# Optimization experiments

Measured on AMD Instinct MI355X. Metric: run time of the kernel, lower is better.

## Reference

```python
import jax, jax.numpy as jnp
import numpy as np

N_ATOMS = 100000
N_BONDS = 250000
MAX_NB = 6
HIDDEN = 256
DEPTH = 3
NUM_MOLS = 2000
ATOM_FDIM = 133
BOND_FDIM = 147


def setup_inputs() -> dict:
    key = jax.random.key(0)
    ks = jax.random.split(key, 12)
    return {
        "f_atoms": jax.random.normal(ks[0], (N_ATOMS, ATOM_FDIM), jnp.float32),
        "f_bonds": jax.random.normal(ks[1], (N_BONDS, BOND_FDIM), jnp.float32),
        "w_atoms": jax.random.uniform(ks[2], (N_ATOMS,), jnp.float32),
        "w_bonds": jax.random.uniform(ks[3], (N_BONDS,), jnp.float32),
        "W_i": jax.random.normal(ks[4], (BOND_FDIM, HIDDEN), jnp.float32) * 0.05,
        "W_h": jax.random.normal(ks[5], (HIDDEN, HIDDEN), jnp.float32) * 0.05,
        "W_o": jax.random.normal(ks[6], (ATOM_FDIM + HIDDEN, HIDDEN), jnp.float32) * 0.05,
        "b_o": jnp.zeros((HIDDEN,), jnp.float32),
        "degree_of_polym": jax.random.uniform(ks[7], (NUM_MOLS,), jnp.float32),
        "a2b": jax.random.randint(ks[8], (N_ATOMS, MAX_NB), 0, N_BONDS, jnp.int32),
        "b2a": jax.random.randint(ks[9], (N_BONDS,), 0, N_ATOMS, jnp.int32),
        "b2revb": jax.random.randint(ks[10], (N_BONDS,), 0, N_BONDS, jnp.int32),
        "mol_ids": jnp.sort(jax.random.randint(ks[11], (N_ATOMS,), 0, NUM_MOLS, jnp.int32)),
    }


def reference(f_atoms, f_bonds, w_atoms, w_bonds, W_i, W_h, W_o, b_o,
              degree_of_polym, a2b, b2a, b2revb, mol_ids):
    # input-layer: bond features -> hidden messages
    inp = f_bonds @ W_i                      # [n_bonds, H]
    message = jax.nn.relu(inp)

    for _ in range(DEPTH - 1):
        # gather incoming bond messages per atom and weight them
        nei_msg = message[a2b]               # [n_atoms, max_nb, H]
        nei_w = w_bonds[a2b]                 # [n_atoms, max_nb]
        a_message = (nei_msg * nei_w[..., None]).sum(axis=1)  # [n_atoms, H]
        # directed message: total at source atom minus reverse bond
        message = a_message[b2a] - message[b2revb]             # [n_bonds, H]
        message = jax.nn.relu(inp + message @ W_h)             # dropout p=0 (eval)

    # final atom-level readout
    nei_msg = message[a2b] * w_bonds[a2b][..., None]
    a_message = nei_msg.sum(axis=1)                            # [n_atoms, H]
    a_input = jnp.concatenate([f_atoms, a_message], axis=1)    # [n_atoms, atom_fdim+H]
    atom_hiddens = jax.nn.relu(a_input @ W_o + b_o)            # [n_atoms, H]

    # per-molecule weighted mean aggregation (a_scope loop -> segment_sum)
    weighted = atom_hiddens * w_atoms[:, None]
    mol_sum = jax.ops.segment_sum(weighted, mol_ids, num_segments=NUM_MOLS)
    w_sum = jax.ops.segment_sum(w_atoms, mol_ids, num_segments=NUM_MOLS)
    safe_w = jnp.where(w_sum > 0, w_sum, 1.0)
    mol_vecs = jnp.where((w_sum > 0)[:, None], mol_sum / safe_w[:, None], 0.0)
    mol_vecs = degree_of_polym[:, None] * mol_vecs             # [num_mols, H]
    return mol_vecs
```

## Files before the change

### kernel.cpp

```cpp
#include <hip/hip_runtime.h>
#include <hip/hip_bf16.h>

typedef unsigned short u16;
typedef __bf16 bf16x8v __attribute__((ext_vector_type(8)));
typedef float f32x4v __attribute__((ext_vector_type(4)));
typedef float f32x4u __attribute__((ext_vector_type(4))) __attribute__((aligned(4)));

__device__ __forceinline__ float bf2f(u16 u) {
    union { float f; unsigned int i; } c; c.i = ((unsigned int)u) << 16; return c.f;
}
__device__ __forceinline__ u16 f2bf(float f) {
    union { float f; unsigned int i; } c; c.f = f;
    unsigned int i = c.i;
    unsigned int lsb = (i >> 16) & 1u;
    i += 0x7fffu + lsb;
    return (u16)(i >> 16);
}
__device__ __forceinline__ float lo16(unsigned u) { return bf2f((u16)(u & 0xffff)); }
__device__ __forceinline__ float hi16(unsigned u) { return bf2f((u16)(u >> 16)); }
__device__ __forceinline__ unsigned pack2(float lo, float hi) {
    return (unsigned)f2bf(lo) | ((unsigned)f2bf(hi) << 16);
}

__device__ __forceinline__ unsigned neg2(unsigned u) { return u ^ 0x80008000u; }
__device__ __forceinline__ unsigned relu_neg2(unsigned u) {
    unsigned s = u & 0x80008000u;
    unsigned m = (s - (s >> 15)) | s;
    return (u ^ 0x80008000u) & ~m;
}

__device__ __forceinline__ bf16x8v load_cvt8(const float* __restrict__ rowp, int k, int kmax) {
    union { unsigned u[4]; bf16x8v v; } r;
#pragma unroll
    for (int g = 0; g < 2; ++g) {
        int kk = k + g * 4;
        float f0, f1, f2, f3;
        if (kk + 3 < kmax) {
            f32x4u q = *(const f32x4u*)(rowp + kk);
            f0 = q.x; f1 = q.y; f2 = q.z; f3 = q.w;
        } else {
            f0 = (kk + 0 < kmax) ? rowp[kk + 0] : 0.f;
            f1 = (kk + 1 < kmax) ? rowp[kk + 1] : 0.f;
            f2 = (kk + 2 < kmax) ? rowp[kk + 2] : 0.f;
            f3 = (kk + 3 < kmax) ? rowp[kk + 3] : 0.f;
        }
        r.u[g * 2]     = pack2(f0, f1);
        r.u[g * 2 + 1] = pack2(f2, f3);
    }
    return r.v;
}

__global__ __launch_bounds__(256)
void pack_all(const float* __restrict__ W_i, const float* __restrict__ W_h,
              const float* __restrict__ W_o,
              u16* __restrict__ wti, u16* __restrict__ wth, u16* __restrict__ wto) {
    int idx = blockIdx.x * 256 + threadIdx.x;
    if (idx < 256 * 160) {
        int n = idx / 160, k = idx % 160;
        wti[idx] = f2bf(k < 147 ? W_i[k * 256 + n] : 0.f);
        return;
    }
    idx -= 256 * 160;
    if (idx < 256 * 256) {
        int n = idx / 256, k = idx % 256;
        wth[idx] = f2bf(W_h[k * 256 + n]);
        return;
    }
    idx -= 256 * 256;
    if (idx < 256 * 448) {
        int n = idx / 448, k = idx % 448;
        float v;
        if (k < 256)       v = W_o[(133 + k) * 256 + n];
        else if (k < 389)  v = W_o[(k - 256) * 256 + n];
        else               v = 0.f;
        wto[idx] = f2bf(v);
    }
}

template <bool RELU>
__global__ __launch_bounds__(256)
void gather16(const u16* __restrict__ msg, const int* __restrict__ a2b,
              const float* __restrict__ w_bonds, u16* __restrict__ out, int nAtoms) {
    int t = threadIdx.x;
    int g = t >> 5;
    int co = (t & 31) * 8;
    int atom0 = blockIdx.x * 16 + g;
    int atom1 = atom0 + 8;
    if (atom1 >= nAtoms) { if (atom0 >= nAtoms) return; atom1 = atom0; }

    int bidx[12];
#pragma unroll
    for (int j = 0; j < 6; ++j) {
        bidx[j]     = a2b[atom0 * 6 + j];
        bidx[6 + j] = a2b[atom1 * 6 + j];
    }
    float w[12];
#pragma unroll
    for (int j = 0; j < 12; ++j) w[j] = w_bonds[bidx[j]];
    uint4 v[12];
#pragma unroll
    for (int j = 0; j < 12; ++j)
        v[j] = *(const uint4*)(msg + (size_t)bidx[j] * 256 + co);

    float a0[8] = {0,0,0,0,0,0,0,0}, a1[8] = {0,0,0,0,0,0,0,0};
#pragma unroll
    for (int j = 0; j < 6; ++j) {
        unsigned p[4] = {v[j].x, v[j].y, v[j].z, v[j].w};
        unsigned q[4] = {v[6+j].x, v[6+j].y, v[6+j].z, v[6+j].w};
#pragma unroll
        for (int c = 0; c < 4; ++c) {
            float m0 = lo16(p[c]), m1 = hi16(p[c]);
            float n0 = lo16(q[c]), n1 = hi16(q[c]);
            if (RELU) {
                m0 = fmaxf(m0, 0.f); m1 = fmaxf(m1, 0.f);
                n0 = fmaxf(n0, 0.f); n1 = fmaxf(n1, 0.f);
            }
            a0[c * 2]     += w[j] * m0;
            a0[c * 2 + 1] += w[j] * m1;
            a1[c * 2]     += w[6+j] * n0;
            a1[c * 2 + 1] += w[6+j] * n1;
        }
    }
    uint4 o0, o1;
    o0.x = pack2(a0[0], a0[1]); o0.y = pack2(a0[2], a0[3]);
    o0.z = pack2(a0[4], a0[5]); o0.w = pack2(a0[6], a0[7]);
    o1.x = pack2(a1[0], a1[1]); o1.y = pack2(a1[2], a1[3]);
    o1.z = pack2(a1[4], a1[5]); o1.w = pack2(a1[6], a1[7]);
    *(uint4*)(out + (size_t)atom0 * 256 + co) = o0;
    if (atom1 != atom0)
        *(uint4*)(out + (size_t)atom1 * 256 + co) = o1;
}

__global__ __launch_bounds__(512, 2)
void gemm_in(const float* __restrict__ A, const u16* __restrict__ Bt, int M,
             u16* __restrict__ out0) {
    constexpr int KPAD = 160, KMAX = 147, ASTR = 147;
    constexpr int LSTR = KPAD + 8;
    __shared__ u16 Bs[256 * LSTR];
    const int tid = threadIdx.x;
    const int wave = tid >> 6;
    const int lane = tid & 63;
    const int mrow = lane & 15;
    const int quad = lane >> 4;

    constexpr int KC = KPAD / 8;
    for (int i = tid; i < 256 * KC; i += 512) {
        int r = i / KC, kc = i % KC;
        *(uint4*)&Bs[r * LSTR + kc * 8] = *(const uint4*)&Bt[(size_t)r * KPAD + kc * 8];
    }
    __syncthreads();

    for (long chunk = blockIdx.x; chunk * 256 < (long)M; chunk += gridDim.x) {
        const long mbase = chunk * 256 + wave * 32;
        const float* rowp[2];
#pragma unroll
        for (int t = 0; t < 2; ++t) {
            long r = mbase + t * 16 + mrow;
            if (r >= M) r = M - 1;
            rowp[t] = A + r * ASTR;
        }

        f32x4v acc[2][16];
#pragma unroll
        for (int t = 0; t < 2; ++t)
#pragma unroll
            for (int j = 0; j < 16; ++j) acc[t][j] = (f32x4v){0.f, 0.f, 0.f, 0.f};

#pragma unroll 2
        for (int k0 = 0; k0 < KPAD; k0 += 32) {
            bf16x8v a_frag[2];
#pragma unroll
            for (int t = 0; t < 2; ++t)
                a_frag[t] = load_cvt8(rowp[t], k0 + quad * 8, KMAX);
#pragma unroll
            for (int jg = 0; jg < 4; ++jg) {
                bf16x8v b_frag[4];
#pragma unroll
                for (int j4 = 0; j4 < 4; ++j4)
                    b_frag[j4] = *(const bf16x8v*)&Bs[((jg * 4 + j4) * 16 + mrow) * LSTR + k0 + quad * 8];
#pragma unroll
                for (int t = 0; t < 2; ++t)
#pragma unroll
                    for (int j4 = 0; j4 < 4; ++j4)
                        acc[t][jg * 4 + j4] = __builtin_amdgcn_mfma_f32_16x16x32_bf16(
                            a_frag[t], b_frag[j4], acc[t][jg * 4 + j4], 0, 0, 0);
            }
        }

#pragma unroll
        for (int t = 0; t < 2; ++t)
#pragma unroll
            for (int r = 0; r < 4; ++r) {
                long grow = mbase + t * 16 + quad * 4 + r;
                if (grow < M)
#pragma unroll
                    for (int j = 0; j < 16; ++j)
                        out0[(size_t)grow * 256 + j * 16 + mrow] = f2bf(acc[t][j][r]);
            }
    }
}

template <bool RELUV>
__global__ __launch_bounds__(512, 4)
void gemm_mp(const u16* __restrict__ amsg, const u16* __restrict__ msgsrc,
             const int* __restrict__ b2a, const int* __restrict__ b2revb,
             const u16* __restrict__ Bt, int M,
             const u16* __restrict__ inp, u16* __restrict__ out0) {
    constexpr int KPAD = 256;
    constexpr int LSTR = KPAD + 8;
    constexpr int NROWS = 128;
    __shared__ u16 Bs[NROWS * LSTR];
    const int tid = threadIdx.x;
    const int wave = tid >> 6;
    const int lane = tid & 63;
    const int mrow = lane & 15;
    const int quad = lane >> 4;

    const int nch = (M + 255) >> 8;
    const int cpx = (nch + 7) >> 3;
    const int bid = blockIdx.x;
    const int xcd = bid & 7;
    const int seq = bid >> 3;
    const long chunk = (long)xcd * cpx + (seq >> 1);
    if (chunk >= nch) return;
    const int nbase = (seq & 1) * NROWS;

    constexpr int KC = KPAD / 8;
    for (int i = tid; i < NROWS * KC; i += 512) {
        int r = i / KC, kc = i % KC;
        *(uint4*)&Bs[r * LSTR + kc * 8] = *(const uint4*)&Bt[(size_t)(nbase + r) * KPAD + kc * 8];
    }
    __syncthreads();

    const long mbase = chunk * 256 + wave * 32;
    size_t soff[2], roff[2];
#pragma unroll
    for (int t = 0; t < 2; ++t) {
        long b = mbase + t * 16 + mrow;
        if (b >= M) b = M - 1;
        soff[t] = (size_t)b2a[b] * 256 + quad * 8;
        roff[t] = (size_t)b2revb[b] * 256 + quad * 8;
    }

    f32x4v acc[2][8];
#pragma unroll
    for (int t = 0; t < 2; ++t)
#pragma unroll
        for (int j = 0; j < 8; ++j) acc[t][j] = (f32x4v){0.f, 0.f, 0.f, 0.f};

    uint4 va[2][2], vr[2][2];
#pragma unroll
    for (int t = 0; t < 2; ++t) {
        va[0][t] = *(const uint4*)&amsg[soff[t]];
        vr[0][t] = *(const uint4*)&msgsrc[roff[t]];
    }
#pragma unroll
    for (int kk = 0; kk < 8; ++kk) {
        const int k0 = kk * 32;
        const int cur = kk & 1, nxt = cur ^ 1;
        if (kk < 7) {
#pragma unroll
            for (int t = 0; t < 2; ++t) {
                va[nxt][t] = *(const uint4*)&amsg[soff[t] + k0 + 32];
                vr[nxt][t] = *(const uint4*)&msgsrc[roff[t] + k0 + 32];
            }
        }
        bf16x8v a1[2], a2[2];
#pragma unroll
        for (int t = 0; t < 2; ++t) {
            union { uint4 q; bf16x8v v; } ua, ur;
            ua.q = va[cur][t];
            uint4 w = vr[cur][t];
            if (RELUV) {
                ur.q.x = relu_neg2(w.x); ur.q.y = relu_neg2(w.y);
                ur.q.z = relu_neg2(w.z); ur.q.w = relu_neg2(w.w);
            } else {
                ur.q.x = neg2(w.x); ur.q.y = neg2(w.y);
                ur.q.z = neg2(w.z); ur.q.w = neg2(w.w);
            }
            a1[t] = ua.v;
            a2[t] = ur.v;
        }
#pragma unroll
        for (int jg = 0; jg < 2; ++jg) {
            bf16x8v b_frag[4];
#pragma unroll
            for (int j4 = 0; j4 < 4; ++j4)
                b_frag[j4] = *(const bf16x8v*)&Bs[((jg * 4 + j4) * 16 + mrow) * LSTR + k0 + quad * 8];
#pragma unroll
            for (int t = 0; t < 2; ++t)
#pragma unroll
                for (int j4 = 0; j4 < 4; ++j4) {
                    acc[t][jg * 4 + j4] = __builtin_amdgcn_mfma_f32_16x16x32_bf16(
                        a1[t], b_frag[j4], acc[t][jg * 4 + j4], 0, 0, 0);
                    acc[t][jg * 4 + j4] = __builtin_amdgcn_mfma_f32_16x16x32_bf16(
                        a2[t], b_frag[j4], acc[t][jg * 4 + j4], 0, 0, 0);
                }
        }
    }

#pragma unroll
    for (int t = 0; t < 2; ++t)
#pragma unroll
        for (int r = 0; r < 4; ++r) {
            long grow = mbase + t * 16 + quad * 4 + r;
            if (grow < M)
#pragma unroll
                for (int j = 0; j < 8; ++j) {
                    size_t idx = (size_t)grow * 256 + nbase + j * 16 + mrow;
                    float s = bf2f(inp[idx]) + acc[t][j][r];
                    out0[idx] = f2bf(s > 0.f ? s : 0.f);
                }
        }
}

__global__ __launch_bounds__(512, 2)
void gemm_ro(const u16* __restrict__ A1, const float* __restrict__ A2,
             const u16* __restrict__ Bt, int M,
             const float* __restrict__ bias, float* __restrict__ outf) {
    constexpr int KPAD = 448, KSPLIT = 256, K2 = 192, KMAX2 = 133;
    constexpr int LSTR = KPAD + 8;
    constexpr int NROWS = 128;
    __shared__ u16 Bs[NROWS * LSTR];
    const int tid = threadIdx.x;
    const int wave = tid >> 6;
    const int lane = tid & 63;
    const int mrow = lane & 15;
    const int quad = lane >> 4;

    const int nch = (M + 255) >> 8;
    const int cpx = (nch + 7) >> 3;
    const int bid = blockIdx.x;
    const int xcd = bid & 7;
    const int seq = bid >> 3;
    const long chunk = (long)xcd * cpx + (seq >> 1);
    if (chunk >= nch) return;
    const int nbase = (seq & 1) * NROWS;

    constexpr int KC = KPAD / 8;
    for (int i = tid; i < NROWS * KC; i += 512) {
        int r = i / KC, kc = i % KC;
        *(uint4*)&Bs[r * LSTR + kc * 8] =
            *(const uint4*)&Bt[(size_t)(nbase + r) * KPAD + kc * 8];
    }
    __syncthreads();

    const long mbase = chunk * 256 + wave * 32;
    long row[2];
#pragma unroll
    for (int t = 0; t < 2; ++t) {
        long r = mbase + t * 16 + mrow;
        if (r >= M) r = M - 1;
        row[t] = r;
    }

    f32x4v acc[2][8];
#pragma unroll
    for (int t = 0; t < 2; ++t)
#pragma unroll
        for (int j = 0; j < 8; ++j) acc[t][j] = (f32x4v){0.f, 0.f, 0.f, 0.f};

#pragma unroll 2
    for (int k0 = 0; k0 < KSPLIT; k0 += 32) {
        bf16x8v a_frag[2], b_frag[8];
#pragma unroll
        for (int t = 0; t < 2; ++t)
            a_frag[t] = *(const bf16x8v*)&A1[row[t] * KSPLIT + k0 + quad * 8];
#pragma unroll
        for (int j = 0; j < 8; ++j)
            b_frag[j] = *(const bf16x8v*)&Bs[(j * 16 + mrow) * LSTR + k0 + quad * 8];
#pragma unroll
        for (int t = 0; t < 2; ++t)
#pragma unroll
            for (int j = 0; j < 8; ++j)
                acc[t][j] = __builtin_amdgcn_mfma_f32_16x16x32_bf16(
                    a_frag[t], b_frag[j], acc[t][j], 0, 0, 0);
    }
#pragma unroll 2
    for (int k0 = 0; k0 < K2; k0 += 32) {
        bf16x8v a_frag[2], b_frag[8];
#pragma unroll
        for (int t = 0; t < 2; ++t)
            a_frag[t] = load_cvt8(A2 + row[t] * KMAX2, k0 + quad * 8, KMAX2);
#pragma unroll
        for (int j = 0; j < 8; ++j)
            b_frag[j] = *(const bf16x8v*)&Bs[(j * 16 + mrow) * LSTR + KSPLIT + k0 + quad * 8];
#pragma unroll
        for (int t = 0; t < 2; ++t)
#pragma unroll
            for (int j = 0; j < 8; ++j)
                acc[t][j] = __builtin_amdgcn_mfma_f32_16x16x32_bf16(
                    a_frag[t], b_frag[j], acc[t][j], 0, 0, 0);
    }

#pragma unroll
    for (int t = 0; t < 2; ++t)
#pragma unroll
        for (int r = 0; r < 4; ++r) {
            long grow = mbase + t * 16 + quad * 4 + r;
            if (grow < M)
#pragma unroll
                for (int j = 0; j < 8; ++j) {
                    int gcol = nbase + j * 16 + mrow;
                    float s = acc[t][j][r] + bias[gcol];
                    outf[(size_t)grow * 256 + gcol] = s > 0.f ? s : 0.f;
                }
        }
}

__global__ __launch_bounds__(256)
void aggregate_kernel(const float* __restrict__ hid, const float* __restrict__ w_atoms,
                      const int* __restrict__ mol_ids, const float* __restrict__ deg,
                      float* __restrict__ out, int nAtoms) {
    int m = blockIdx.x;
    int t = threadIdx.x;
    int lo = 0, hi = nAtoms;
    while (lo < hi) { int mid = (lo + hi) >> 1; if (mol_ids[mid] < m) lo = mid + 1; else hi = mid; }
    int start = lo;
    lo = start; hi = nAtoms;
    while (lo < hi) { int mid = (lo + hi) >> 1; if (mol_ids[mid] < m + 1) lo = mid + 1; else hi = mid; }
    int end = lo;
    float acc = 0.f, wsum = 0.f;
    for (int a = start; a < end; ++a) {
        float w = w_atoms[a];
        wsum += w;
        acc += w * hid[(size_t)a * 256 + t];
    }
    float res = (wsum > 0.f) ? deg[m] * acc / wsum : 0.f;
    out[m * 256 + t] = res;
}

extern "C" void kernel_launch(void* const* d_in, const int* in_sizes, int n_in,
                              void* d_out, int out_size, void* d_ws, size_t ws_size,
                              hipStream_t stream) {
    const float* f_atoms = (const float*)d_in[0];
    const float* f_bonds = (const float*)d_in[1];
    const float* w_atoms = (const float*)d_in[2];
    const float* w_bonds = (const float*)d_in[3];
    const float* W_i     = (const float*)d_in[4];
    const float* W_h     = (const float*)d_in[5];
    const float* W_o     = (const float*)d_in[6];
    const float* b_o     = (const float*)d_in[7];
    const float* deg     = (const float*)d_in[8];
    const int*   a2b     = (const int*)d_in[9];
    const int*   b2a     = (const int*)d_in[10];
    const int*   b2revb  = (const int*)d_in[11];
    const int*   mol_ids = (const int*)d_in[12];
    float* out = (float*)d_out;

    const int nB = 250000, nA = 100000, nM = 2000;

    char* ws = (char*)d_ws;
    u16* inp    = (u16*)(ws);
    u16* msgA   = (u16*)(ws + 128000000L);
    float* hid  = (float*)(ws + 256000000L);
    u16* amsg   = (u16*)(ws + 384000000L);
    u16* wt_i   = (u16*)(ws + 435200000L);
    u16* wt_h   = (u16*)(ws + 435200000L + 81920L);
    u16* wt_o   = (u16*)(ws + 435200000L + 81920L + 131072L);

    if (ws_size < 435642368UL) return;

    dim3 b256(256), b512(512);
    pack_all<<<dim3((256 * 160 + 256 * 256 + 256 * 448 + 255) / 256), b256, 0, stream>>>(
        W_i, W_h, W_o, wt_i, wt_h, wt_o);

    gemm_in<<<dim3(977), b512, 0, stream>>>(f_bonds, wt_i, nB, inp);

    const int nchB = (nB + 255) >> 8, cpxB = (nchB + 7) >> 3;
    dim3 gmp(8 * cpxB * 2);
    const int nchA = (nA + 255) >> 8, cpxA = (nchA + 7) >> 3;
    dim3 gro(8 * cpxA * 2);

    gather16<true><<<dim3((nA + 15) / 16), b256, 0, stream>>>(inp, a2b, w_bonds, amsg, nA);
    gemm_mp<true><<<gmp, b512, 0, stream>>>(
        amsg, inp, b2a, b2revb, wt_h, nB, inp, msgA);

    gather16<false><<<dim3((nA + 15) / 16), b256, 0, stream>>>(msgA, a2b, w_bonds, amsg, nA);
    gemm_mp<false><<<gmp, b512, 0, stream>>>(
        amsg, msgA, b2a, b2revb, wt_h, nB, inp, inp);

    gather16<false><<<dim3((nA + 15) / 16), b256, 0, stream>>>(inp , a2b, w_bonds, amsg, nA);
    gemm_ro<<<gro, b512, 0, stream>>>(amsg, f_atoms, wt_o, nA, b_o, hid);

    aggregate_kernel<<<dim3(nM), b256, 0, stream>>>(hid, w_atoms, mol_ids, deg, out, nA);
}
```

Measured before the change: 902.5 us.

## Retile message-passing GEMM to 1024-thread blocks holding all of W_h in LDS

Rewrites gemm_mp so each 1024-thread block stages the full 256x256 W_h in shared memory and covers 128 bond rows. Pairs of waves share a 16-row tile and each wave takes one half of the output columns. The XCD-aware chunk mapping and the register double-buffered prefetch of gathered rows are dropped in favour of a simple unroll-2 K loop. This halves per-wave accumulators and may raise latency hiding, but each LDS B fragment now feeds one row tile instead of two. Each block also copies twice as much weight data into LDS, and both waves in a pair gather the same A rows.

```diff
diff --git a/kernel.cpp b/kernel.cpp
--- a/kernel.cpp
+++ b/kernel.cpp
@@ -201,117 +201,70 @@
 }
 
 template <bool RELUV>
-__global__ __launch_bounds__(512, 4)
+__global__ __launch_bounds__(1024, 4)
 void gemm_mp(const u16* __restrict__ amsg, const u16* __restrict__ msgsrc,
              const int* __restrict__ b2a, const int* __restrict__ b2revb,
              const u16* __restrict__ Bt, int M,
              const u16* __restrict__ inp, u16* __restrict__ out0) {
     constexpr int KPAD = 256;
     constexpr int LSTR = KPAD + 8;
-    constexpr int NROWS = 128;
-    __shared__ u16 Bs[NROWS * LSTR];
+    __shared__ u16 Bs[256 * LSTR];
     const int tid = threadIdx.x;
     const int wave = tid >> 6;
     const int lane = tid & 63;
     const int mrow = lane & 15;
     const int quad = lane >> 4;
-
-    const int nch = (M + 255) >> 8;
-    const int cpx = (nch + 7) >> 3;
-    const int bid = blockIdx.x;
-    const int xcd = bid & 7;
-    const int seq = bid >> 3;
-    const long chunk = (long)xcd * cpx + (seq >> 1);
-    if (chunk >= nch) return;
-    const int nbase = (seq & 1) * NROWS;
-
-    constexpr int KC = KPAD / 8;
-    for (int i = tid; i < NROWS * KC; i += 512) {
-        int r = i / KC, kc = i % KC;
-        *(uint4*)&Bs[r * LSTR + kc * 8] = *(const uint4*)&Bt[(size_t)(nbase + r) * KPAD + kc * 8];
+    const int wgrp = wave >> 1;
+    const int nbase = (wave & 1) * 128;
+
+    for (int i = tid; i < 256 * 32; i += 1024) {
+        int r = i >> 5, kc = i & 31;
+        *(uint4*)&Bs[r * LSTR + kc * 8] = *(const uint4*)&Bt[(size_t)r * KPAD + kc * 8];
     }
     __syncthreads();
 
-    const long mbase = chunk * 256 + wave * 32;
-    size_t soff[2], roff[2];
-#pragma unroll
-    for (int t = 0; t < 2; ++t) {
-        long b = mbase + t * 16 + mrow;
-        if (b >= M) b = M - 1;
-        soff[t] = (size_t)b2a[b] * 256 + quad * 8;
-        roff[t] = (size_t)b2revb[b] * 256 + quad * 8;
-    }
-
-    f32x4v acc[2][8];
-#pragma unroll
-    for (int t = 0; t < 2; ++t)
-#pragma unroll
-        for (int j = 0; j < 8; ++j) acc[t][j] = (f32x4v){0.f, 0.f, 0.f, 0.f};
-
-    uint4 va[2][2], vr[2][2];
-#pragma unroll
-    for (int t = 0; t < 2; ++t) {
-        va[0][t] = *(const uint4*)&amsg[soff[t]];
-        vr[0][t] = *(const uint4*)&msgsrc[roff[t]];
-    }
-#pragma unroll
-    for (int kk = 0; kk < 8; ++kk) {
-        const int k0 = kk * 32;
-        const int cur = kk & 1, nxt = cur ^ 1;
-        if (kk < 7) {
-#pragma unroll
-            for (int t = 0; t < 2; ++t) {
-                va[nxt][t] = *(const uint4*)&amsg[soff[t] + k0 + 32];
-                vr[nxt][t] = *(const uint4*)&msgsrc[roff[t] + k0 + 32];
+    const long mbase = (long)blockIdx.x * 128 + wgrp * 16;
+    long b = mbase + mrow;
+    if (b >= M) b = M - 1;
+    const size_t soff = (size_t)b2a[b] * 256 + quad * 8;
+    const size_t roff = (size_t)b2revb[b] * 256 + quad * 8;
+
+    f32x4v acc[8];
+#pragma unroll
+    for (int j = 0; j < 8; ++j) acc[j] = (f32x4v){0.f, 0.f, 0.f, 0.f};
+
+#pragma unroll 2
+    for (int k0 = 0; k0 < KPAD; k0 += 32) {
+        uint4 va = *(const uint4*)&amsg[soff + k0];
+        uint4 vr = *(const uint4*)&msgsrc[roff + k0];
+        union { uint4 q; bf16x8v v; } ua, ur;
+        ua.q = va;
+        if (RELUV) {
+            ur.q.x = relu_neg2(vr.x); ur.q.y = relu_neg2(vr.y);
+            ur.q.z = relu_neg2(vr.z); ur.q.w = relu_neg2(vr.w);
+        } else {
+            ur.q.x = neg2(vr.x); ur.q.y = neg2(vr.y);
+            ur.q.z = neg2(vr.z); ur.q.w = neg2(vr.w);
+        }
+#pragma unroll
+        for (int j = 0; j < 8; ++j) {
+            bf16x8v b_frag = *(const bf16x8v*)&Bs[(nbase + j * 16 + mrow) * LSTR + k0 + quad * 8];
+            acc[j] = __builtin_amdgcn_mfma_f32_16x16x32_bf16(ua.v, b_frag, acc[j], 0, 0, 0);
+            acc[j] = __builtin_amdgcn_mfma_f32_16x16x32_bf16(ur.v, b_frag, acc[j], 0, 0, 0);
+        }
+    }
+
+#pragma unroll
+    for (int r = 0; r < 4; ++r) {
+        long grow = mbase + quad * 4 + r;
+        if (grow < M)
+#pragma unroll
+            for (int j = 0; j < 8; ++j) {
+                size_t idx = (size_t)grow * 256 + nbase + j * 16 + mrow;
+                float s = bf2f(inp[idx]) + acc[j][r];
+                out0[idx] = f2bf(s > 0.f ? s : 0.f);
             }
-        }
-        bf16x8v a1[2], a2[2];
-#pragma unroll
-        for (int t = 0; t < 2; ++t) {
-            union { uint4 q; bf16x8v v; } ua, ur;
-            ua.q = va[cur][t];
-            uint4 w = vr[cur][t];
-            if (RELUV) {
-                ur.q.x = relu_neg2(w.x); ur.q.y = relu_neg2(w.y);
-                ur.q.z = relu_neg2(w.z); ur.q.w = relu_neg2(w.w);
-            } else {
-                ur.q.x = neg2(w.x); ur.q.y = neg2(w.y);
-                ur.q.z = neg2(w.z); ur.q.w = neg2(w.w);
-            }
-            a1[t] = ua.v;
-            a2[t] = ur.v;
-        }
-#pragma unroll
-        for (int jg = 0; jg < 2; ++jg) {
-            bf16x8v b_frag[4];
-#pragma unroll
-            for (int j4 = 0; j4 < 4; ++j4)
-                b_frag[j4] = *(const bf16x8v*)&Bs[((jg * 4 + j4) * 16 + mrow) * LSTR + k0 + quad * 8];
-#pragma unroll
-            for (int t = 0; t < 2; ++t)
-#pragma unroll
-                for (int j4 = 0; j4 < 4; ++j4) {
-                    acc[t][jg * 4 + j4] = __builtin_amdgcn_mfma_f32_16x16x32_bf16(
-                        a1[t], b_frag[j4], acc[t][jg * 4 + j4], 0, 0, 0);
-                    acc[t][jg * 4 + j4] = __builtin_amdgcn_mfma_f32_16x16x32_bf16(
-                        a2[t], b_frag[j4], acc[t][jg * 4 + j4], 0, 0, 0);
-                }
-        }
-    }
-
-#pragma unroll
-    for (int t = 0; t < 2; ++t)
-#pragma unroll
-        for (int r = 0; r < 4; ++r) {
-            long grow = mbase + t * 16 + quad * 4 + r;
-            if (grow < M)
-#pragma unroll
-                for (int j = 0; j < 8; ++j) {
-                    size_t idx = (size_t)grow * 256 + nbase + j * 16 + mrow;
-                    float s = bf2f(inp[idx]) + acc[t][j][r];
-                    out0[idx] = f2bf(s > 0.f ? s : 0.f);
-                }
-        }
+    }
 }
 
 __global__ __launch_bounds__(512, 2)
@@ -461,23 +414,22 @@
 
     if (ws_size < 435642368UL) return;
 
-    dim3 b256(256), b512(512);
+    dim3 b256(256), b512(512), b1024(1024);
     pack_all<<<dim3((256 * 160 + 256 * 256 + 256 * 448 + 255) / 256), b256, 0, stream>>>(
         W_i, W_h, W_o, wt_i, wt_h, wt_o);
 
     gemm_in<<<dim3(977), b512, 0, stream>>>(f_bonds, wt_i, nB, inp);
 
-    const int nchB = (nB + 255) >> 8, cpxB = (nchB + 7) >> 3;
-    dim3 gmp(8 * cpxB * 2);
+    dim3 gmp((nB + 127) / 128);
     const int nchA = (nA + 255) >> 8, cpxA = (nchA + 7) >> 3;
     dim3 gro(8 * cpxA * 2);
 
     gather16<true><<<dim3((nA + 15) / 16), b256, 0, stream>>>(inp, a2b, w_bonds, amsg, nA);
-    gemm_mp<true><<<gmp, b512, 0, stream>>>(
+    gemm_mp<true><<<gmp, b1024, 0, stream>>>(
         amsg, inp, b2a, b2revb, wt_h, nB, inp, msgA);
 
     gather16<false><<<dim3((nA + 15) / 16), b256, 0, stream>>>(msgA, a2b, w_bonds, amsg, nA);
-    gemm_mp<false><<<gmp, b512, 0, stream>>>(
+    gemm_mp<false><<<gmp, b1024, 0, stream>>>(
         amsg, msgA, b2a, b2revb, wt_h, nB, inp, inp);
 
     gather16<false><<<dim3((nA + 15) / 16), b256, 0, stream>>>(inp , a2b, w_bonds, amsg, nA);
```

Result: faster. 857.8 us (-5.0%).
